# Kernel tuning notes

Measured on AMD Instinct MI355X. Metric: run time of the kernel, lower is better.

The kernel has to match this reference:

```python
import jax, jax.numpy as jnp
import numpy as np

B, T = 8, 512
N_QUBITS, N_ROT, D_PER = 64, 16, 64
D = N_QUBITS * D_PER


def setup_inputs() -> dict:
    key = jax.random.key(0)
    k1, k2, k3, k4 = jax.random.split(key, 4)
    return {
        "x": jax.random.normal(k1, (B, T, D), dtype=jnp.float32),
        "rx_params": jax.random.normal(k2, (N_QUBITS, N_ROT), dtype=jnp.float32),
        "ry_params": jax.random.normal(k3, (N_QUBITS, N_ROT), dtype=jnp.float32),
        "rz_params": jax.random.normal(k4, (N_QUBITS, N_ROT), dtype=jnp.float32),
    }


def _rot_diag(theta, axis):
    # theta: (Q,) per-qubit angle. The torch einsum 'btqd,btqq->btqd' only uses
    # the diagonal of the (Q,Q) rotation matrix. For rx/ry, the paired-qubit
    # construction puts cos(theta_k/2) on both diagonal slots of pair k
    # (first Q//2 angles are used, matching cos[..., :len(idx)]).
    Q = theta.shape[0]
    half = theta[: Q // 2] * 0.5
    if axis in ("x", "y"):
        return jnp.repeat(jnp.cos(half).astype(jnp.complex64), 2)
    # rz: diag(exp(-i a/2), exp(+i a/2)) interleaved over pairs
    e = jnp.exp(-1j * half.astype(jnp.complex64))
    return jnp.stack([e, jnp.conj(e)], axis=-1).reshape(-1)


def _apply_rotation(state, theta, axis):
    # state: (B, T, Q, d_per) complex64
    sf = jnp.fft.fft2(state, axes=(-2, -1))
    sf = sf * _rot_diag(theta, axis)[:, None]  # diagonal per-qubit scale
    return jnp.fft.ifft2(sf, axes=(-2, -1)).real  # torch takes .real


def reference(x, rx_params, ry_params, rz_params):
    b, t, d = x.shape
    q = rx_params.shape[0]
    state = x.reshape(b, t, q, d // q).astype(jnp.complex64)
    for params, axis in ((rx_params, "x"), (ry_params, "y"), (rz_params, "z")):
        theta = params.sum(-1)  # combine n_rotations into one angle per qubit
        state = _apply_rotation(state, theta, axis).astype(jnp.complex64)
    state = state.reshape(b, t, d)
    # noise model: (1 + amp_noise) * exp(i * phase_noise) * state, then L2 norm
    ka, kp = jax.random.split(jax.random.key(42))
    amp = 0.01 * jax.random.normal(ka, state.shape, dtype=jnp.float32)
    ph = 0.005 * jax.random.normal(kp, state.shape, dtype=jnp.float32)
    noisy = (1.0 + amp) * jnp.exp(1j * ph.astype(jnp.complex64)) * state
    norm = jnp.linalg.norm(noisy, axis=-1, keepdims=True)
    noisy = noisy / (norm + 1e-8)
    return jnp.abs(noisy)  # measurement
```

## Files before the change

kernel.cpp:

```cpp
#include <hip/hip_runtime.h>
#include <hip/hip_bf16.h>
#include <stdint.h>

__device__ __forceinline__ uint32_t rotl32(uint32_t v, int r) {
  return (v << r) | (v >> (32 - r));
}

__device__ __forceinline__ void threefry2x32(uint32_t k0, uint32_t k1,
                                             uint32_t x0, uint32_t x1,
                                             uint32_t& o0, uint32_t& o1) {
  uint32_t k2 = k0 ^ k1 ^ 0x1BD11BDAu;
  x0 += k0; x1 += k1;
#define TF_R(r) { x0 += x1; x1 = rotl32(x1, (r)); x1 ^= x0; }
  TF_R(13) TF_R(15) TF_R(26) TF_R(6)   x0 += k1; x1 += k2 + 1u;
  TF_R(17) TF_R(29) TF_R(16) TF_R(24)  x0 += k2; x1 += k0 + 2u;
  TF_R(13) TF_R(15) TF_R(26) TF_R(6)   x0 += k0; x1 += k1 + 3u;
  TF_R(17) TF_R(29) TF_R(16) TF_R(24)  x0 += k1; x1 += k2 + 4u;
  TF_R(13) TF_R(15) TF_R(26) TF_R(6)   x0 += k2; x1 += k0 + 5u;
#undef TF_R
  o0 = x0; o1 = x1;
}

__device__ __forceinline__ float erfinv_fast(float x) {
  float w = -__logf(fmaf(-x, x, 1.0f));
  float p;
  if (w < 5.0f) {
    w = w - 2.5f;
    p = 2.81022636e-08f;
    p = fmaf(p, w, 3.43273939e-07f);
    p = fmaf(p, w, -3.5233877e-06f);
    p = fmaf(p, w, -4.39150654e-06f);
    p = fmaf(p, w, 0.00021858087f);
    p = fmaf(p, w, -0.00125372503f);
    p = fmaf(p, w, -0.00417768164f);
    p = fmaf(p, w, 0.246640727f);
    p = fmaf(p, w, 1.50140941f);
  } else {
    w = sqrtf(w) - 3.0f;
    p = -0.000200214257f;
    p = fmaf(p, w, 0.000100950558f);
    p = fmaf(p, w, 0.00134934322f);
    p = fmaf(p, w, -0.00367342844f);
    p = fmaf(p, w, 0.00573950773f);
    p = fmaf(p, w, -0.0076224613f);
    p = fmaf(p, w, 0.00943887047f);
    p = fmaf(p, w, 1.00167406f);
    p = fmaf(p, w, 2.83297682f);
  }
  return p * x;
}

__device__ __align__(16) float g_coeff[64];
__device__ uint32_t g_key[2];

__global__ void setup_kernel(const float* __restrict__ rx,
                             const float* __restrict__ ry,
                             const float* __restrict__ rz) {
  __shared__ float cre[3][64], cim[3][64];
  __shared__ float Gr[64], Gi[64];
  __shared__ float twc[64], tws[64];
  const int t = threadIdx.x;

  if (t < 32) {
    const float* ps[3] = {rx, ry, rz};
    for (int a = 0; a < 3; ++a) {
      float s = 0.0f;
      for (int r = 0; r < 16; ++r) s += ps[a][t * 16 + r];
      float h = 0.5f * s;
      float ch = cosf(h), sh = sinf(h);
      if (a < 2) {
        cre[a][2 * t] = ch;     cim[a][2 * t] = 0.0f;
        cre[a][2 * t + 1] = ch; cim[a][2 * t + 1] = 0.0f;
      } else {
        cre[2][2 * t] = ch;     cim[2][2 * t] = -sh;
        cre[2][2 * t + 1] = ch; cim[2][2 * t + 1] = sh;
      }
    }
  }
  {
    double ang = (2.0 * 3.14159265358979323846 / 64.0) * (double)t;
    twc[t] = (float)cos(ang);
    tws[t] = (float)sin(ang);
  }
  __syncthreads();

  {
    const int k = t, kn = (64 - k) & 63;
    float pr = 1.0f, pi = 0.0f;
    for (int a = 0; a < 3; ++a) {
      float cr = 0.5f * (cre[a][k] + cre[a][kn]);
      float ci = 0.5f * (cim[a][k] - cim[a][kn]);
      float nr = pr * cr - pi * ci;
      float ni = pr * ci + pi * cr;
      pr = nr; pi = ni;
    }
    Gr[k] = pr; Gi[k] = pi;
  }
  __syncthreads();

  {
    const int m = t;
    float s = 0.0f;
    for (int k = 0; k < 64; ++k) {
      int idx = (k * m) & 63;
      s = fmaf(Gr[k], twc[idx], s);
      s = fmaf(-Gi[k], tws[idx], s);
    }
    g_coeff[m] = s * (1.0f / 64.0f);
  }

  if (t == 0) {
    uint32_t o0, o1;
    threefry2x32(0u, 42u, 0u, 0u, o0, o1);
    g_key[0] = o0; g_key[1] = o1;
  }
}

__global__ __launch_bounds__(256, 5) void qmain(const float* __restrict__ x,
                                                float* __restrict__ out) {
  __shared__ float Xs[4096];
  __shared__ float red[4];
  const int tid = threadIdx.x;
  const int row = blockIdx.x;

  {
    const float4* xin = (const float4*)(x + (size_t)row * 4096);
    float4* xs4 = (float4*)Xs;
#pragma unroll
    for (int k = 0; k < 4; ++k) xs4[tid + k * 256] = xin[tid + k * 256];
  }

  const int d = tid & 63;
  const int qb = (tid >> 6) * 16;
  const int qbu = __builtin_amdgcn_readfirstlane(qb);

  float G[64];
  {
    const float4* g4 = (const float4*)g_coeff;
    const int rot = qbu >> 2;
#pragma unroll
    for (int k = 0; k < 16; ++k) {
      float4 v = g4[(k + rot) & 15];
      G[4 * k + 0] = v.x; G[4 * k + 1] = v.y; G[4 * k + 2] = v.z; G[4 * k + 3] = v.w;
    }
  }
  const uint32_t ka0 = g_key[0], ka1 = g_key[1];

  __syncthreads();

  float acc[16];
#pragma unroll
  for (int j = 0; j < 16; ++j) acc[j] = 0.0f;

#pragma unroll
  for (int p = 0; p < 64; ++p) {
    float xv = Xs[(p << 6) + d];
#pragma unroll
    for (int j = 0; j < 16; ++j) acc[j] = fmaf(G[(j - p) & 63], xv, acc[j]);
  }

  __syncthreads();
#pragma unroll
  for (int j = 0; j < 16; ++j) Xs[((qb + j) << 6) + d] = acc[j];
  __syncthreads();

  const uint32_t base = ((uint32_t)row << 12) + (uint32_t)tid;
  float wabs[16];
  float ssum = 0.0f;
#pragma unroll
  for (int k = 0; k < 16; ++k) {
    const uint32_t idx = base + ((uint32_t)k << 8);
    uint32_t o0, o1;
    threefry2x32(ka0, ka1, 0u, idx, o0, o1);
    uint32_t bits = o0 ^ o1;
    float f = __uint_as_float((bits >> 9) | 0x3f800000u) - 1.0f;
    const float lo = -0.99999994f;
    float u = fmaxf(fmaf(f, 2.0f, lo), lo);
    float z = 1.41421356237309515f * erfinv_fast(u);
    float w = fmaf(0.01f, z, 1.0f) * Xs[tid + (k << 8)];
    ssum = fmaf(w, w, ssum);
    wabs[k] = fabsf(w);
  }

#pragma unroll
  for (int off = 32; off >= 1; off >>= 1) ssum += __shfl_xor(ssum, off, 64);
  if ((tid & 63) == 0) red[tid >> 6] = ssum;
  __syncthreads();
  const float total = red[0] + red[1] + red[2] + red[3];
  const float scale = 1.0f / (sqrtf(total) + 1e-8f);

  float* orow = out + (size_t)row * 4096;
#pragma unroll
  for (int k = 0; k < 16; ++k) orow[tid + (k << 8)] = wabs[k] * scale;
}

extern "C" void kernel_launch(void* const* d_in, const int* in_sizes, int n_in,
                              void* d_out, int out_size, void* d_ws, size_t ws_size,
                              hipStream_t stream) {
  const float* x  = (const float*)d_in[0];
  const float* rx = (const float*)d_in[1];
  const float* ry = (const float*)d_in[2];
  const float* rz = (const float*)d_in[3];
  float* out = (float*)d_out;

  setup_kernel<<<1, 64, 0, stream>>>(rx, ry, rz);
  qmain<<<4096, 256, 0, stream>>>(x, out);
}
```

Before: 152.7 us.

## Compute circulant qubit mixing with fp16 MFMA instead of scalar FMAs

Replaces the per-thread 64x16 scalar FMA circulant convolution over the qubit axis with MFMA 16x16x32 fp16 matrix multiplies. The input row is converted to fp16 and stored transposed, with padding, in shared memory, and the circulant coefficients are precomputed reversed and duplicated in fp16. The noise and normalization stage then consumes the MFMA accumulator layout directly, which removes a shared-memory round trip and one barrier. Rounding inputs and coefficients to fp16 lowers precision, and the transposed shared-memory stores may cause bank conflicts.

```diff
diff --git a/kernel.cpp b/kernel.cpp
--- a/kernel.cpp
+++ b/kernel.cpp
@@ -1,6 +1,8 @@
 #include <hip/hip_runtime.h>
-#include <hip/hip_bf16.h>
 #include <stdint.h>
+
+typedef _Float16 half8 __attribute__((ext_vector_type(8)));
+typedef float floatx4 __attribute__((ext_vector_type(4)));
 
 __device__ __forceinline__ uint32_t rotl32(uint32_t v, int r) {
   return (v << r) | (v >> (32 - r));
@@ -50,7 +52,7 @@
   return p * x;
 }
 
-__device__ __align__(16) float g_coeff[64];
+__device__ __align__(16) _Float16 grevh2[128];
 __device__ uint32_t g_key[2];
 
 __global__ void setup_kernel(const float* __restrict__ rx,
@@ -59,6 +61,7 @@
   __shared__ float cre[3][64], cim[3][64];
   __shared__ float Gr[64], Gi[64];
   __shared__ float twc[64], tws[64];
+  __shared__ float gs[64];
   const int t = threadIdx.x;
 
   if (t < 32) {
@@ -99,14 +102,21 @@
   __syncthreads();
 
   {
-    const int m = t;
+    const int mi = t;
     float s = 0.0f;
     for (int k = 0; k < 64; ++k) {
-      int idx = (k * m) & 63;
+      int idx = (k * mi) & 63;
       s = fmaf(Gr[k], twc[idx], s);
       s = fmaf(-Gi[k], tws[idx], s);
     }
-    g_coeff[m] = s * (1.0f / 64.0f);
+    gs[mi] = s * (1.0f / 64.0f);
+  }
+  __syncthreads();
+
+  {
+    _Float16 hv = (_Float16)gs[(64 - t) & 63];
+    grevh2[t] = hv;
+    grevh2[t + 64] = hv;
   }
 
   if (t == 0) {
@@ -118,80 +128,93 @@
 
 __global__ __launch_bounds__(256, 5) void qmain(const float* __restrict__ x,
                                                 float* __restrict__ out) {
-  __shared__ float Xs[4096];
+  __shared__ __align__(16) _Float16 Xt[64 * 72];
   __shared__ float red[4];
   const int tid = threadIdx.x;
   const int row = blockIdx.x;
-
-  {
-    const float4* xin = (const float4*)(x + (size_t)row * 4096);
-    float4* xs4 = (float4*)Xs;
-#pragma unroll
-    for (int k = 0; k < 4; ++k) xs4[tid + k * 256] = xin[tid + k * 256];
-  }
-
-  const int d = tid & 63;
-  const int qb = (tid >> 6) * 16;
-  const int qbu = __builtin_amdgcn_readfirstlane(qb);
-
-  float G[64];
-  {
-    const float4* g4 = (const float4*)g_coeff;
-    const int rot = qbu >> 2;
-#pragma unroll
-    for (int k = 0; k < 16; ++k) {
-      float4 v = g4[(k + rot) & 15];
-      G[4 * k + 0] = v.x; G[4 * k + 1] = v.y; G[4 * k + 2] = v.z; G[4 * k + 3] = v.w;
-    }
+  const int lane = tid & 63;
+  const int w = tid >> 6;
+  const int quad = lane >> 4;
+  const int m = lane & 15;
+
+  half8 af0, af1;
+  {
+    const int s0 = (8 * quad - 16 * w - m) & 63;
+    const int s1 = (32 + 8 * quad - 16 * w - m) & 63;
+#pragma unroll
+    for (int j = 0; j < 8; ++j) af0[j] = grevh2[s0 + j];
+#pragma unroll
+    for (int j = 0; j < 8; ++j) af1[j] = grevh2[s1 + j];
   }
   const uint32_t ka0 = g_key[0], ka1 = g_key[1];
 
-  __syncthreads();
-
-  float acc[16];
-#pragma unroll
-  for (int j = 0; j < 16; ++j) acc[j] = 0.0f;
-
-#pragma unroll
-  for (int p = 0; p < 64; ++p) {
-    float xv = Xs[(p << 6) + d];
-#pragma unroll
-    for (int j = 0; j < 16; ++j) acc[j] = fmaf(G[(j - p) & 63], xv, acc[j]);
-  }
-
-  __syncthreads();
-#pragma unroll
-  for (int j = 0; j < 16; ++j) Xs[((qb + j) << 6) + d] = acc[j];
-  __syncthreads();
-
-  const uint32_t base = ((uint32_t)row << 12) + (uint32_t)tid;
+  {
+    const float* xr = x + (size_t)row * 4096;
+    const int tq = tid >> 4;
+    const int d0 = (tid & 15) * 4;
+#pragma unroll
+    for (int u = 0; u < 2; ++u) {
+      const int q0 = 2 * tq + 32 * u;
+      float4 a = *(const float4*)(xr + q0 * 64 + d0);
+      float4 b = *(const float4*)(xr + (q0 + 1) * 64 + d0);
+      const float av[4] = {a.x, a.y, a.z, a.w};
+      const float bv[4] = {b.x, b.y, b.z, b.w};
+#pragma unroll
+      for (int i = 0; i < 4; ++i) {
+        union { _Float16 h[2]; uint32_t u32; } pk;
+        pk.h[0] = (_Float16)av[i];
+        pk.h[1] = (_Float16)bv[i];
+        *(uint32_t*)&Xt[(d0 + i) * 72 + q0] = pk.u32;
+      }
+    }
+  }
+  __syncthreads();
+
+  floatx4 acc[4];
+#pragma unroll
+  for (int c = 0; c < 4; ++c) {
+    const _Float16* bp = &Xt[(16 * c + m) * 72 + 8 * quad];
+    half8 b0 = *(const half8*)bp;
+    half8 b1 = *(const half8*)(bp + 32);
+    acc[c] = (floatx4){0.0f, 0.0f, 0.0f, 0.0f};
+    acc[c] = __builtin_amdgcn_mfma_f32_16x16x32_f16(af0, b0, acc[c], 0, 0, 0);
+    acc[c] = __builtin_amdgcn_mfma_f32_16x16x32_f16(af1, b1, acc[c], 0, 0, 0);
+  }
+
+  const uint32_t idxbase = ((uint32_t)row << 12) + (uint32_t)(((16 * w + 4 * quad) << 6) + m);
   float wabs[16];
   float ssum = 0.0f;
 #pragma unroll
-  for (int k = 0; k < 16; ++k) {
-    const uint32_t idx = base + ((uint32_t)k << 8);
-    uint32_t o0, o1;
-    threefry2x32(ka0, ka1, 0u, idx, o0, o1);
-    uint32_t bits = o0 ^ o1;
-    float f = __uint_as_float((bits >> 9) | 0x3f800000u) - 1.0f;
-    const float lo = -0.99999994f;
-    float u = fmaxf(fmaf(f, 2.0f, lo), lo);
-    float z = 1.41421356237309515f * erfinv_fast(u);
-    float w = fmaf(0.01f, z, 1.0f) * Xs[tid + (k << 8)];
-    ssum = fmaf(w, w, ssum);
-    wabs[k] = fabsf(w);
+  for (int c = 0; c < 4; ++c) {
+#pragma unroll
+    for (int r = 0; r < 4; ++r) {
+      const uint32_t idx = idxbase + (uint32_t)(r * 64 + 16 * c);
+      uint32_t o0, o1;
+      threefry2x32(ka0, ka1, 0u, idx, o0, o1);
+      uint32_t bits = o0 ^ o1;
+      float f = __uint_as_float((bits >> 9) | 0x3f800000u) - 1.0f;
+      const float lo = -0.99999994f;
+      float u = fmaxf(fmaf(f, 2.0f, lo), lo);
+      float z = 1.41421356237309515f * erfinv_fast(u);
+      float wv = fmaf(0.01f, z, 1.0f) * acc[c][r];
+      ssum = fmaf(wv, wv, ssum);
+      wabs[c * 4 + r] = fabsf(wv);
+    }
   }
 
 #pragma unroll
   for (int off = 32; off >= 1; off >>= 1) ssum += __shfl_xor(ssum, off, 64);
-  if ((tid & 63) == 0) red[tid >> 6] = ssum;
+  if (lane == 0) red[w] = ssum;
   __syncthreads();
   const float total = red[0] + red[1] + red[2] + red[3];
   const float scale = 1.0f / (sqrtf(total) + 1e-8f);
 
-  float* orow = out + (size_t)row * 4096;
-#pragma unroll
-  for (int k = 0; k < 16; ++k) orow[tid + (k << 8)] = wabs[k] * scale;
+  float* ob = out + (size_t)row * 4096 + (size_t)(((16 * w + 4 * quad) << 6) + m);
+#pragma unroll
+  for (int c = 0; c < 4; ++c)
+#pragma unroll
+    for (int r = 0; r < 4; ++r)
+      ob[r * 64 + 16 * c] = wabs[c * 4 + r] * scale;
 }
 
 extern "C" void kernel_launch(void* const* d_in, const int* in_sizes, int n_in,
```

After: 142.6 us. 6.6% less time.
